# Kernel optimization log

Measured on AMD Instinct MI355X. Metric: run time of the kernel, lower is better.

The kernel has to match this reference:

```python
import jax, jax.numpy as jnp
import numpy as np

THETA = 10.0      # neuron['theta']
TAU_SR = 10.0     # neuron['tauSr']
TAU_REF = 1.0     # neuron['tauRef']
SCALE_REF = 2.0   # neuron['scaleRef']
TAU_RHO = 1.0     # neuron['tauRho']
SCALE_RHO = 1.0   # neuron['scaleRho']
EPS = 0.01        # kernel truncation epsilon
TS = 1.0          # simulation['Ts']
T_SAMPLE = 256    # time steps == seq_len (forward sets tSample = embed_out.size(1))


def _alpha_kernel(tau, mult):
    # slayerPytorch _calculateAlphaKernel: mult * t/tau * exp(1 - t/tau), truncated
    ker = []
    for t in np.arange(0.0, T_SAMPLE * TS, TS):
        v = mult * t / tau * np.exp(1.0 - t / tau)
        if abs(v) < EPS and t > tau:
            break
        ker.append(v)
    return np.asarray(ker, dtype=np.float32)


def psp(x, srm_kernel):
    # Causal temporal filter: out[t] = Ts * sum_k srm[k] * x[t-k];  x: (B, C, T)
    B, C, T = x.shape
    K = srm_kernel.shape[0]
    lhs = x.reshape(B * C, 1, T)
    rhs = srm_kernel[::-1].reshape(1, 1, K)  # reverse: correlation -> convolution
    out = jax.lax.conv_general_dilated(lhs, rhs, (1,), [(K - 1, 0)])
    return out.reshape(B, C, T) * TS


def _spike_scan(u, ref_kernel):
    # Sequential threshold with refractory feedback (SLAYER getSpikes). u: (B, C, T)
    B, C, T = u.shape
    future = ref_kernel[1:]  # ref_kernel[0] == 0, so spike at t only affects t+1..
    R = future.shape[0]

    def step(r, u_t):
        m = u_t + r[..., 0]                       # membrane incl. past refractory
        s = (m >= THETA).astype(u.dtype)
        r = jnp.concatenate([r[..., 1:], jnp.zeros_like(r[..., :1])], axis=-1)
        r = r + s[..., None] * future             # schedule refractory response
        return r, (s, m)

    r0 = jnp.zeros((B, C, R), u.dtype)
    _, (s, m) = jax.lax.scan(step, r0, jnp.moveaxis(u, -1, 0))
    return jnp.moveaxis(s, 0, -1), jnp.moveaxis(m, 0, -1)


@jax.custom_vjp
def spike(u, ref_kernel):
    return _spike_scan(u, ref_kernel)[0]


def _spike_fwd(u, ref_kernel):
    s, m = _spike_scan(u, ref_kernel)
    return s, (m, ref_kernel)


def _spike_bwd(res, g):
    # SLAYER surrogate gradient: straight-through pdf on post-refractory membrane
    m, ref_kernel = res
    tau = TAU_RHO * THETA
    pdf = (SCALE_RHO / tau) * jnp.exp(-jnp.abs(m - THETA) / tau)
    return g * pdf, jnp.zeros_like(ref_kernel)


spike.defvjp(_spike_fwd, _spike_bwd)


def setup_inputs() -> dict:
    key = jax.random.key(0)
    k1, k2, k3, k4 = jax.random.split(key, 4)
    VOCAB, EMB, HID, OUT, B = 50000, 300, 512, 10, 64
    feed_data = jax.random.randint(k1, (B, T_SAMPLE), 0, VOCAB)
    emb_weight = jax.random.normal(k2, (VOCAB, EMB), jnp.float32)
    W1 = jax.random.normal(k3, (HID, EMB), jnp.float32) * (4.0 / np.sqrt(EMB))
    W2 = jax.random.normal(k4, (OUT, HID), jnp.float32) * (4.0 / np.sqrt(HID))
    return {
        "feed_data": feed_data,
        "emb_weight": emb_weight,
        "W1": W1,
        "W2": W2,
        "srm_kernel": jnp.asarray(_alpha_kernel(TAU_SR, 1.0)),
        "ref_kernel": jnp.asarray(_alpha_kernel(TAU_REF, -SCALE_REF * THETA)),
    }


def reference(feed_data, emb_weight, W1, W2, srm_kernel, ref_kernel):
    x = emb_weight[feed_data]                 # (B, T, E); dropout = identity (eval)
    x = jnp.transpose(x, (0, 2, 1))           # (B, E, T) -- transpose(1,2)
    h = jnp.einsum('he,bet->bht', W1, x)      # slayer.dense == 1x1x1 conv3d, no bias
    h = spike(psp(h, srm_kernel), ref_kernel)
    o = jnp.einsum('oh,bht->bot', W2, h)
    return spike(psp(o, srm_kernel), ref_kernel)  # (B, OUT, T)
```

## Files before the change

### kernel.cpp

```cpp
#include <hip/hip_runtime.h>

#define BB   64
#define TT   256
#define EMBD 300
#define HIDD 512
#define OUTC 10
#define CT   16
#define THETA 10.0
#define FUTN 12

struct S1A { float x[TT][33]; float w[CT][32]; };
struct S1B { double h[CT][257]; float s[CT][257]; };
union  SmemL1 { S1A a; S1B b; };

__global__ __launch_bounds__(256)
void layer1_kernel(const int* __restrict__ feed, const float* __restrict__ emb,
                   const float* __restrict__ W1, const float* __restrict__ srm,
                   const float* __restrict__ refk, float* __restrict__ s1,
                   int Ks, int Kr)
{
    __shared__ SmemL1 sm;
    __shared__ int    idxb[TT];
    __shared__ double srm_sm[TT];

    const int tid = threadIdx.x;
    const int b   = blockIdx.x;
    const int c0  = blockIdx.y * CT;

    idxb[tid]   = feed[b * TT + tid];
    srm_sm[tid] = (tid < Ks) ? (double)srm[tid] : 0.0;
    __syncthreads();

    double acc[CT];
#pragma unroll
    for (int c = 0; c < CT; ++c) acc[c] = 0.0;

    const int e_lane = tid & 31;
    const int t_row  = tid >> 5;

    for (int e0 = 0; e0 < EMBD; e0 += 32) {
        const int ec = min(32, EMBD - e0);
        if (e_lane < ec) {
#pragma unroll
            for (int p = 0; p < 32; ++p) {
                const int t = t_row + (p << 3);
                sm.a.x[t][e_lane] = emb[(size_t)idxb[t] * EMBD + e0 + e_lane];
            }
        }
        for (int j = tid; j < CT * 32; j += 256) {
            const int c = j >> 5, ee = j & 31;
            if (ee < ec) sm.a.w[c][ee] = W1[(size_t)(c0 + c) * EMBD + e0 + ee];
        }
        __syncthreads();
        for (int e = 0; e < ec; ++e) {
            const double xv = (double)sm.a.x[tid][e];
#pragma unroll
            for (int c = 0; c < CT; ++c)
                acc[c] = fma(xv, (double)sm.a.w[c][e], acc[c]);
        }
        __syncthreads();
    }

#pragma unroll
    for (int c = 0; c < CT; ++c) sm.b.h[c][tid] = acc[c];
    __syncthreads();

    double p2[CT];
#pragma unroll
    for (int c = 0; c < CT; ++c) p2[c] = 0.0;
    const int jmax = min(tid, Ks - 1);
    for (int j = 0; j <= jmax; ++j) {
        const double sj = srm_sm[j];
#pragma unroll
        for (int c = 0; c < CT; ++c)
            p2[c] = fma(sm.b.h[c][tid - j], sj, p2[c]);
    }
    __syncthreads();
#pragma unroll
    for (int c = 0; c < CT; ++c) sm.b.h[c][tid] = p2[c];
    __syncthreads();

    if (tid < CT) {
        double fut[FUTN];
#pragma unroll
        for (int i = 0; i < FUTN; ++i)
            fut[i] = (i + 1 < Kr) ? (double)refk[i + 1] : 0.0;
        double r[FUTN];
#pragma unroll
        for (int i = 0; i < FUTN; ++i) r[i] = 0.0;
        for (int t = 0; t < TT; ++t) {
            const double m  = sm.b.h[tid][t] + r[0];
            const double sv = (m >= THETA) ? 1.0 : 0.0;
#pragma unroll
            for (int i = 0; i < FUTN - 1; ++i) r[i] = fma(sv, fut[i], r[i + 1]);
            r[FUTN - 1] = sv * fut[FUTN - 1];
            sm.b.s[tid][t] = (float)sv;
        }
    }
    __syncthreads();
#pragma unroll
    for (int c = 0; c < CT; ++c)
        s1[((size_t)b * HIDD + c0 + c) * TT + tid] = sm.b.s[c][tid];
}

struct S2B { double h[OUTC][257]; float s[OUTC][257]; };
union  SmemL2 { float w[OUTC][HIDD]; S2B b; };

__global__ __launch_bounds__(256)
void layer2_kernel(const float* __restrict__ s1, const float* __restrict__ W2,
                   const float* __restrict__ srm, const float* __restrict__ refk,
                   float* __restrict__ out, int Ks, int Kr)
{
    __shared__ SmemL2 sm;
    __shared__ double srm_sm[TT];

    const int tid = threadIdx.x;
    const int b   = blockIdx.x;

    srm_sm[tid] = (tid < Ks) ? (double)srm[tid] : 0.0;
    for (int j = tid; j < OUTC * HIDD; j += 256) ((float*)sm.w)[j] = W2[j];
    __syncthreads();

    double acc[OUTC];
#pragma unroll
    for (int oc = 0; oc < OUTC; ++oc) acc[oc] = 0.0;

    const float* srow = s1 + (size_t)b * HIDD * TT + tid;
#pragma unroll 4
    for (int h = 0; h < HIDD; ++h) {
        const double sv = (double)srow[(size_t)h * TT];
#pragma unroll
        for (int oc = 0; oc < OUTC; ++oc)
            acc[oc] = fma(sv, (double)sm.w[oc][h], acc[oc]);
    }
    __syncthreads();

#pragma unroll
    for (int oc = 0; oc < OUTC; ++oc) sm.b.h[oc][tid] = acc[oc];
    __syncthreads();

    double p2[OUTC];
#pragma unroll
    for (int oc = 0; oc < OUTC; ++oc) p2[oc] = 0.0;
    const int jmax = min(tid, Ks - 1);
    for (int j = 0; j <= jmax; ++j) {
        const double sj = srm_sm[j];
#pragma unroll
        for (int oc = 0; oc < OUTC; ++oc)
            p2[oc] = fma(sm.b.h[oc][tid - j], sj, p2[oc]);
    }
    __syncthreads();
#pragma unroll
    for (int oc = 0; oc < OUTC; ++oc) sm.b.h[oc][tid] = p2[oc];
    __syncthreads();

    if (tid < OUTC) {
        double fut[FUTN];
#pragma unroll
        for (int i = 0; i < FUTN; ++i)
            fut[i] = (i + 1 < Kr) ? (double)refk[i + 1] : 0.0;
        double r[FUTN];
#pragma unroll
        for (int i = 0; i < FUTN; ++i) r[i] = 0.0;
        for (int t = 0; t < TT; ++t) {
            const double m  = sm.b.h[tid][t] + r[0];
            const double sv = (m >= THETA) ? 1.0 : 0.0;
#pragma unroll
            for (int i = 0; i < FUTN - 1; ++i) r[i] = fma(sv, fut[i], r[i + 1]);
            r[FUTN - 1] = sv * fut[FUTN - 1];
            sm.b.s[tid][t] = (float)sv;
        }
    }
    __syncthreads();
#pragma unroll
    for (int oc = 0; oc < OUTC; ++oc)
        out[((size_t)b * OUTC + oc) * TT + tid] = sm.b.s[oc][tid];
}

extern "C" void kernel_launch(void* const* d_in, const int* in_sizes, int n_in,
                              void* d_out, int out_size, void* d_ws, size_t ws_size,
                              hipStream_t stream)
{
    const int*   feed = (const int*)  d_in[0];
    const float* emb  = (const float*)d_in[1];
    const float* W1   = (const float*)d_in[2];
    const float* W2   = (const float*)d_in[3];
    const float* srm  = (const float*)d_in[4];
    const float* refk = (const float*)d_in[5];
    const int Ks = in_sizes[4];
    const int Kr = in_sizes[5];

    float* s1  = (float*)d_ws;
    float* out = (float*)d_out;

    layer1_kernel<<<dim3(BB, HIDD / CT), 256, 0, stream>>>(
        feed, emb, W1, srm, refk, s1, Ks, Kr);
    layer2_kernel<<<dim3(BB), 256, 0, stream>>>(
        s1, W2, srm, refk, out, Ks, Kr);
}
```

Baseline: 416.2 us.

## Restructure SNN pipeline: pre-gather embeddings, register-tiled GEMM, windowed PSP, byte spikes

Adds a prep kernel that gathers and transposes embedding rows into an (B,E,T) buffer and converts W2 to double. Layer1 switches to a 4x4 register-tiled double GEMM with double-buffered register prefetch. The PSP convolution is truncated to KSMAX taps using a sliding-window register scheme over swizzled shared memory. Hidden spikes are stored as bytes instead of floats, so layer2 reads a quarter of the data. The costs are an extra launch and workspace round trip for the gathered input, and a hardcoded assumption that the SRM kernel has at most 80 taps.

```diff
diff --git a/kernel.cpp b/kernel.cpp
--- a/kernel.cpp
+++ b/kernel.cpp
@@ -1,180 +1,311 @@
 #include <hip/hip_runtime.h>
 
-#define BB   64
-#define TT   256
-#define EMBD 300
-#define HIDD 512
-#define OUTC 10
-#define CT   16
+#define BB    64
+#define TT    256
+#define EMBD  300
+#define HIDD  512
+#define OUTC  10
 #define THETA 10.0
-#define FUTN 12
-
-struct S1A { float x[TT][33]; float w[CT][32]; };
-struct S1B { double h[CT][257]; float s[CT][257]; };
-union  SmemL1 { S1A a; S1B b; };
+#define FUTN  12
+#define KSMAX 80
+#define HSTRIDE 344
+
+__device__ __forceinline__ int hswz(int tt) { return tt ^ ((tt >> 4) & 7); }
 
 __global__ __launch_bounds__(256)
-void layer1_kernel(const int* __restrict__ feed, const float* __restrict__ emb,
-                   const float* __restrict__ W1, const float* __restrict__ srm,
-                   const float* __restrict__ refk, float* __restrict__ s1,
-                   int Ks, int Kr)
+void prep_kernel(const int* __restrict__ feed, const float* __restrict__ emb,
+                 const float* __restrict__ W2, float* __restrict__ xg,
+                 double* __restrict__ w2d)
 {
-    __shared__ SmemL1 sm;
-    __shared__ int    idxb[TT];
-    __shared__ double srm_sm[TT];
-
+    if (blockIdx.y == 8) {
+        const int k = blockIdx.x * 256 + threadIdx.x;
+        if (k < OUTC * HIDD) w2d[k] = (double)W2[k];
+        return;
+    }
+    __shared__ float xt[32][305];
+    __shared__ int   idx32[32];
     const int tid = threadIdx.x;
     const int b   = blockIdx.x;
-    const int c0  = blockIdx.y * CT;
-
-    idxb[tid]   = feed[b * TT + tid];
-    srm_sm[tid] = (tid < Ks) ? (double)srm[tid] : 0.0;
-    __syncthreads();
-
-    double acc[CT];
-#pragma unroll
-    for (int c = 0; c < CT; ++c) acc[c] = 0.0;
-
-    const int e_lane = tid & 31;
-    const int t_row  = tid >> 5;
-
-    for (int e0 = 0; e0 < EMBD; e0 += 32) {
-        const int ec = min(32, EMBD - e0);
-        if (e_lane < ec) {
-#pragma unroll
-            for (int p = 0; p < 32; ++p) {
-                const int t = t_row + (p << 3);
-                sm.a.x[t][e_lane] = emb[(size_t)idxb[t] * EMBD + e0 + e_lane];
+    const int t0  = blockIdx.y * 32;
+
+    if (tid < 32) idx32[tid] = feed[b * TT + t0 + tid];
+    __syncthreads();
+    for (int t = tid >> 6; t < 32; t += 4) {
+        const size_t row = (size_t)idx32[t] * EMBD;
+        for (int e = (tid & 63); e < EMBD; e += 64)
+            xt[t][e] = emb[row + e];
+    }
+    __syncthreads();
+    const int tl = tid & 7;
+    for (int e = tid >> 3; e < EMBD; e += 32) {
+        float4 v;
+        v.x = xt[4 * tl + 0][e];
+        v.y = xt[4 * tl + 1][e];
+        v.z = xt[4 * tl + 2][e];
+        v.w = xt[4 * tl + 3][e];
+        *(float4*)&xg[((size_t)b * EMBD + e) * TT + t0 + 4 * tl] = v;
+    }
+}
+
+__global__ __launch_bounds__(256, 3)
+void layer1_kernel(const float* __restrict__ xg, const float* __restrict__ W1,
+                   const float* __restrict__ srm, const float* __restrict__ refk,
+                   unsigned char* __restrict__ s1, int Ks, int Kr)
+{
+    __shared__ union {
+        float  x[16 * 260];
+        double h[16 * HSTRIDE];
+    } A;
+    __shared__ union {
+        double        w[16 * 34];
+        unsigned char s[16 * 260];
+    } B;
+    __shared__ double srm_sm[KSMAX];
+
+    const int tid = threadIdx.x;
+    const int b   = blockIdx.x;
+    const int c0  = blockIdx.y * 16;
+
+    if (tid < KSMAX) srm_sm[tid] = (tid < Ks) ? (double)srm[tid] : 0.0;
+
+    const int cg = tid & 3,  tg = tid >> 2;
+    const int tl = tid & 63, wv = tid >> 6;
+    const int ew = tid & 15, cw = tid >> 4;
+
+    double acc[4][4];
+#pragma unroll
+    for (int i = 0; i < 4; ++i)
+#pragma unroll
+        for (int j = 0; j < 4; ++j) acc[i][j] = 0.0;
+
+    float xr[4][4];
+    float wr = 0.f;
+
+    {
+#pragma unroll
+        for (int r = 0; r < 4; ++r)
+            *(float4*)xr[r] = *(const float4*)&xg[((size_t)b * EMBD + 4 * wv + r) * TT + 4 * tl];
+        wr = W1[(size_t)(c0 + cw) * EMBD + ew];
+#pragma unroll
+        for (int r = 0; r < 4; ++r)
+            *(float4*)&A.x[(4 * wv + r) * 260 + 4 * tl] = *(float4*)xr[r];
+        B.w[ew * 34 + cw] = (double)wr;
+    }
+    __syncthreads();
+
+    const int NCH = (EMBD + 15) / 16;
+    for (int ch = 0; ch < NCH; ++ch) {
+        const int ecur = min(16, EMBD - ch * 16);
+        const int e0n  = (ch + 1) * 16;
+        const int ecn  = EMBD - e0n;
+        if (ch + 1 < NCH) {
+#pragma unroll
+            for (int r = 0; r < 4; ++r) {
+                const int e = 4 * wv + r;
+                if (e < ecn)
+                    *(float4*)xr[r] = *(const float4*)&xg[((size_t)b * EMBD + e0n + e) * TT + 4 * tl];
             }
-        }
-        for (int j = tid; j < CT * 32; j += 256) {
-            const int c = j >> 5, ee = j & 31;
-            if (ee < ec) sm.a.w[c][ee] = W1[(size_t)(c0 + c) * EMBD + e0 + ee];
+            if (ew < ecn) wr = W1[(size_t)(c0 + cw) * EMBD + e0n + ew];
+        }
+        const float*  xp = &A.x[4 * tg];
+        const double* wp = &B.w[4 * cg];
+#pragma unroll 4
+        for (int e = 0; e < ecur; ++e) {
+            const float4  xv = *(const float4*)xp;
+            const double2 wa = *(const double2*)wp;
+            const double2 wb = *(const double2*)(wp + 2);
+            const double xd0 = (double)xv.x, xd1 = (double)xv.y;
+            const double xd2 = (double)xv.z, xd3 = (double)xv.w;
+            acc[0][0] = fma(xd0, wa.x, acc[0][0]);
+            acc[0][1] = fma(xd0, wa.y, acc[0][1]);
+            acc[0][2] = fma(xd0, wb.x, acc[0][2]);
+            acc[0][3] = fma(xd0, wb.y, acc[0][3]);
+            acc[1][0] = fma(xd1, wa.x, acc[1][0]);
+            acc[1][1] = fma(xd1, wa.y, acc[1][1]);
+            acc[1][2] = fma(xd1, wb.x, acc[1][2]);
+            acc[1][3] = fma(xd1, wb.y, acc[1][3]);
+            acc[2][0] = fma(xd2, wa.x, acc[2][0]);
+            acc[2][1] = fma(xd2, wa.y, acc[2][1]);
+            acc[2][2] = fma(xd2, wb.x, acc[2][2]);
+            acc[2][3] = fma(xd2, wb.y, acc[2][3]);
+            acc[3][0] = fma(xd3, wa.x, acc[3][0]);
+            acc[3][1] = fma(xd3, wa.y, acc[3][1]);
+            acc[3][2] = fma(xd3, wb.x, acc[3][2]);
+            acc[3][3] = fma(xd3, wb.y, acc[3][3]);
+            xp += 260;
+            wp += 34;
         }
         __syncthreads();
-        for (int e = 0; e < ec; ++e) {
-            const double xv = (double)sm.a.x[tid][e];
-#pragma unroll
-            for (int c = 0; c < CT; ++c)
-                acc[c] = fma(xv, (double)sm.a.w[c][e], acc[c]);
-        }
-        __syncthreads();
-    }
-
-#pragma unroll
-    for (int c = 0; c < CT; ++c) sm.b.h[c][tid] = acc[c];
-    __syncthreads();
-
-    double p2[CT];
-#pragma unroll
-    for (int c = 0; c < CT; ++c) p2[c] = 0.0;
-    const int jmax = min(tid, Ks - 1);
-    for (int j = 0; j <= jmax; ++j) {
-        const double sj = srm_sm[j];
-#pragma unroll
-        for (int c = 0; c < CT; ++c)
-            p2[c] = fma(sm.b.h[c][tid - j], sj, p2[c]);
-    }
-    __syncthreads();
-#pragma unroll
-    for (int c = 0; c < CT; ++c) sm.b.h[c][tid] = p2[c];
-    __syncthreads();
-
-    if (tid < CT) {
-        double fut[FUTN];
-#pragma unroll
-        for (int i = 0; i < FUTN; ++i)
+        if (ch + 1 < NCH) {
+#pragma unroll
+            for (int r = 0; r < 4; ++r) {
+                const int e = 4 * wv + r;
+                if (e < ecn)
+                    *(float4*)&A.x[e * 260 + 4 * tl] = *(float4*)xr[r];
+            }
+            if (ew < ecn) B.w[ew * 34 + cw] = (double)wr;
+            __syncthreads();
+        }
+    }
+
+    const int cf = tid & 15, tb = tid >> 4;
+    if (tb < 5) {
+#pragma unroll
+        for (int k = 0; k < 16; ++k)
+            A.h[cf * HSTRIDE + hswz(tb * 16 + k)] = 0.0;
+    }
+#pragma unroll
+    for (int i = 0; i < 4; ++i)
+#pragma unroll
+        for (int j = 0; j < 4; ++j)
+            A.h[(4 * cg + j) * HSTRIDE + hswz(80 + 4 * tg + i)] = acc[i][j];
+    __syncthreads();
+
+    const int t0f = tb * 16;
+    double* hrow = &A.h[cf * HSTRIDE];
+    double p[16], win[16];
+#pragma unroll
+    for (int k = 0; k < 16; ++k) {
+        p[k]   = 0.0;
+        win[k] = hrow[hswz(80 + t0f + k)];
+    }
+    for (int jb = 0; jb < KSMAX; jb += 16) {
+#pragma unroll
+        for (int jj = 0; jj < 16; ++jj) {
+            const double sj = srm_sm[jb + jj];
+#pragma unroll
+            for (int i = 0; i < 16; ++i)
+                p[i] = fma(win[(16 + i - jj) & 15], sj, p[i]);
+            win[(15 - jj) & 15] = hrow[hswz(80 + t0f - (jb + jj) - 1)];
+        }
+    }
+    __syncthreads();
+#pragma unroll
+    for (int i = 0; i < 16; ++i)
+        hrow[hswz(80 + t0f + i)] = p[i];
+    __syncthreads();
+
+    if (tid < 16) {
+        double fut[FUTN], rsh[FUTN];
+#pragma unroll
+        for (int i = 0; i < FUTN; ++i) {
             fut[i] = (i + 1 < Kr) ? (double)refk[i + 1] : 0.0;
-        double r[FUTN];
-#pragma unroll
-        for (int i = 0; i < FUTN; ++i) r[i] = 0.0;
+            rsh[i] = 0.0;
+        }
+        const double*  hr = &A.h[tid * HSTRIDE];
+        unsigned char* sr = &B.s[tid * 260];
         for (int t = 0; t < TT; ++t) {
-            const double m  = sm.b.h[tid][t] + r[0];
+            const double m  = hr[hswz(80 + t)] + rsh[0];
             const double sv = (m >= THETA) ? 1.0 : 0.0;
 #pragma unroll
-            for (int i = 0; i < FUTN - 1; ++i) r[i] = fma(sv, fut[i], r[i + 1]);
-            r[FUTN - 1] = sv * fut[FUTN - 1];
-            sm.b.s[tid][t] = (float)sv;
-        }
-    }
-    __syncthreads();
-#pragma unroll
-    for (int c = 0; c < CT; ++c)
-        s1[((size_t)b * HIDD + c0 + c) * TT + tid] = sm.b.s[c][tid];
+            for (int i = 0; i < FUTN - 1; ++i) rsh[i] = fma(sv, fut[i], rsh[i + 1]);
+            rsh[FUTN - 1] = sv * fut[FUTN - 1];
+            sr[t] = (unsigned char)(sv != 0.0 ? 1 : 0);
+        }
+    }
+    __syncthreads();
+
+    {
+        const int tl2 = tid & 63;
+#pragma unroll
+        for (int r = 0; r < 4; ++r) {
+            const int c = (tid >> 6) + 4 * r;
+            const unsigned int v = *(const unsigned int*)&B.s[c * 260 + 4 * tl2];
+            *(unsigned int*)&s1[((size_t)b * HIDD + c0 + c) * TT + 4 * tl2] = v;
+        }
+    }
 }
 
-struct S2B { double h[OUTC][257]; float s[OUTC][257]; };
-union  SmemL2 { float w[OUTC][HIDD]; S2B b; };
-
 __global__ __launch_bounds__(256)
-void layer2_kernel(const float* __restrict__ s1, const float* __restrict__ W2,
+void layer2_kernel(const unsigned char* __restrict__ s1,
+                   const double* __restrict__ w2d,
                    const float* __restrict__ srm, const float* __restrict__ refk,
                    float* __restrict__ out, int Ks, int Kr)
 {
-    __shared__ SmemL2 sm;
-    __shared__ double srm_sm[TT];
+    __shared__ double        h2[OUTC * HSTRIDE];
+    __shared__ unsigned char s2[OUTC * 260];
+    __shared__ double        srm_sm[KSMAX];
 
     const int tid = threadIdx.x;
     const int b   = blockIdx.x;
 
-    srm_sm[tid] = (tid < Ks) ? (double)srm[tid] : 0.0;
-    for (int j = tid; j < OUTC * HIDD; j += 256) ((float*)sm.w)[j] = W2[j];
-    __syncthreads();
+    if (tid < KSMAX) srm_sm[tid] = (tid < Ks) ? (double)srm[tid] : 0.0;
 
     double acc[OUTC];
 #pragma unroll
     for (int oc = 0; oc < OUTC; ++oc) acc[oc] = 0.0;
 
-    const float* srow = s1 + (size_t)b * HIDD * TT + tid;
-#pragma unroll 4
+    const unsigned char* sp = s1 + (size_t)b * HIDD * TT + tid;
+#pragma unroll 8
     for (int h = 0; h < HIDD; ++h) {
-        const double sv = (double)srow[(size_t)h * TT];
+        const double sv = (double)sp[(size_t)h * TT];
 #pragma unroll
         for (int oc = 0; oc < OUTC; ++oc)
-            acc[oc] = fma(sv, (double)sm.w[oc][h], acc[oc]);
-    }
-    __syncthreads();
-
-#pragma unroll
-    for (int oc = 0; oc < OUTC; ++oc) sm.b.h[oc][tid] = acc[oc];
-    __syncthreads();
-
-    double p2[OUTC];
-#pragma unroll
-    for (int oc = 0; oc < OUTC; ++oc) p2[oc] = 0.0;
-    const int jmax = min(tid, Ks - 1);
-    for (int j = 0; j <= jmax; ++j) {
-        const double sj = srm_sm[j];
-#pragma unroll
-        for (int oc = 0; oc < OUTC; ++oc)
-            p2[oc] = fma(sm.b.h[oc][tid - j], sj, p2[oc]);
-    }
-    __syncthreads();
-#pragma unroll
-    for (int oc = 0; oc < OUTC; ++oc) sm.b.h[oc][tid] = p2[oc];
+            acc[oc] = fma(sv, w2d[oc * HIDD + h], acc[oc]);
+    }
+
+    const int cf = tid & 15, tb = tid >> 4;
+    if (cf < OUTC && tb < 5) {
+#pragma unroll
+        for (int k = 0; k < 16; ++k)
+            h2[cf * HSTRIDE + hswz(tb * 16 + k)] = 0.0;
+    }
+#pragma unroll
+    for (int oc = 0; oc < OUTC; ++oc)
+        h2[oc * HSTRIDE + hswz(80 + tid)] = acc[oc];
+    __syncthreads();
+
+    double p[16], win[16];
+    double* hrow = &h2[cf * HSTRIDE];
+    const int t0f = tb * 16;
+    if (cf < OUTC) {
+#pragma unroll
+        for (int k = 0; k < 16; ++k) {
+            p[k]   = 0.0;
+            win[k] = hrow[hswz(80 + t0f + k)];
+        }
+        for (int jb = 0; jb < KSMAX; jb += 16) {
+#pragma unroll
+            for (int jj = 0; jj < 16; ++jj) {
+                const double sj = srm_sm[jb + jj];
+#pragma unroll
+                for (int i = 0; i < 16; ++i)
+                    p[i] = fma(win[(16 + i - jj) & 15], sj, p[i]);
+                win[(15 - jj) & 15] = hrow[hswz(80 + t0f - (jb + jj) - 1)];
+            }
+        }
+    }
+    __syncthreads();
+    if (cf < OUTC) {
+#pragma unroll
+        for (int i = 0; i < 16; ++i)
+            hrow[hswz(80 + t0f + i)] = p[i];
+    }
     __syncthreads();
 
     if (tid < OUTC) {
-        double fut[FUTN];
-#pragma unroll
-        for (int i = 0; i < FUTN; ++i)
+        double fut[FUTN], rsh[FUTN];
+#pragma unroll
+        for (int i = 0; i < FUTN; ++i) {
             fut[i] = (i + 1 < Kr) ? (double)refk[i + 1] : 0.0;
-        double r[FUTN];
-#pragma unroll
-        for (int i = 0; i < FUTN; ++i) r[i] = 0.0;
+            rsh[i] = 0.0;
+        }
+        const double*  hr = &h2[tid * HSTRIDE];
+        unsigned char* sr = &s2[tid * 260];
         for (int t = 0; t < TT; ++t) {
-            const double m  = sm.b.h[tid][t] + r[0];
+            const double m  = hr[hswz(80 + t)] + rsh[0];
             const double sv = (m >= THETA) ? 1.0 : 0.0;
 #pragma unroll
-            for (int i = 0; i < FUTN - 1; ++i) r[i] = fma(sv, fut[i], r[i + 1]);
-            r[FUTN - 1] = sv * fut[FUTN - 1];
-            sm.b.s[tid][t] = (float)sv;
-        }
-    }
-    __syncthreads();
-#pragma unroll
-    for (int oc = 0; oc < OUTC; ++oc)
-        out[((size_t)b * OUTC + oc) * TT + tid] = sm.b.s[oc][tid];
+            for (int i = 0; i < FUTN - 1; ++i) rsh[i] = fma(sv, fut[i], rsh[i + 1]);
+            rsh[FUTN - 1] = sv * fut[FUTN - 1];
+            sr[t] = (unsigned char)(sv != 0.0 ? 1 : 0);
+        }
+    }
+    __syncthreads();
+
+#pragma unroll
+    for (int r = 0; r < OUTC; ++r)
+        out[((size_t)b * OUTC + r) * TT + tid] = (float)s2[r * 260 + tid];
 }
 
 extern "C" void kernel_launch(void* const* d_in, const int* in_sizes, int n_in,
@@ -190,11 +321,12 @@
     const int Ks = in_sizes[4];
     const int Kr = in_sizes[5];
 
-    float* s1  = (float*)d_ws;
-    float* out = (float*)d_out;
-
-    layer1_kernel<<<dim3(BB, HIDD / CT), 256, 0, stream>>>(
-        feed, emb, W1, srm, refk, s1, Ks, Kr);
-    layer2_kernel<<<dim3(BB), 256, 0, stream>>>(
-        s1, W2, srm, refk, out, Ks, Kr);
+    unsigned char* s1c = (unsigned char*)d_ws;
+    float*  xg  = (float*) ((char*)d_ws + 8388608);
+    double* w2d = (double*)((char*)d_ws + 8388608 + 19660800);
+    float*  out = (float*)d_out;
+
+    prep_kernel  <<<dim3(BB, 9),  256, 0, stream>>>(feed, emb, W2, xg, w2d);
+    layer1_kernel<<<dim3(BB, 32), 256, 0, stream>>>(xg, W1, srm, refk, s1c, Ks, Kr);
+    layer2_kernel<<<dim3(BB),     256, 0, stream>>>(s1c, w2d, srm, refk, out, Ks, Kr);
 }
```

After: 382.9 us. -8.0%, faster.
